# Kernel tuning notes

Hardware: AMD Instinct MI355X
Metric: run time of the kernel (lower is better)

Reference implementation:

```python
import jax, jax.numpy as jnp
import numpy as np

N_NODES = 150000
M_HYPEREDGES = 50000
N_TOTAL = N_NODES + M_HYPEREDGES
LATENT_DIM = 64
NUM_CLASS = 50
NNZ = 3_200_000
NUM_LAYERS = 3


def setup_inputs() -> dict:
    key = jax.random.key(0)
    k1, k2, k3, k4, k5, k6 = jax.random.split(key, 6)
    node_emb = 0.1 * jax.random.normal(k1, (N_NODES, LATENT_DIM), dtype=jnp.float32)
    hyper_emb = 0.1 * jax.random.normal(k2, (M_HYPEREDGES, LATENT_DIM), dtype=jnp.float32)
    W = jax.random.normal(k3, (LATENT_DIM, NUM_CLASS), dtype=jnp.float32) / np.sqrt(LATENT_DIM)
    b = jnp.zeros((NUM_CLASS,), dtype=jnp.float32)
    rows = jax.random.randint(k4, (NNZ,), 0, N_TOTAL, dtype=jnp.int32)
    cols = jax.random.randint(k5, (NNZ,), 0, N_TOTAL, dtype=jnp.int32)
    # normalized-adjacency-like small positive values
    vals = jax.random.uniform(k6, (NNZ,), dtype=jnp.float32) * 0.1
    return {"node_emb": node_emb, "hyper_emb": hyper_emb, "W": W, "b": b,
            "vals": vals, "rows": rows, "cols": cols}


def _spmm(vals, rows, cols, x):
    # y[r] = sum over edges (r, c): vals * x[c]   -- COO SpMM
    return jax.ops.segment_sum(vals[:, None] * x[cols], rows, num_segments=N_TOTAL)


def reference(node_emb, hyper_emb, W, b, vals, rows, cols):
    all_emb = jnp.concatenate([node_emb, hyper_emb], axis=0)  # [N, D]
    acc = all_emb  # running sum across layer embeddings (fused mean-pool)
    for _ in range(NUM_LAYERS):
        all_emb = _spmm(vals, rows, cols, all_emb)
        acc = acc + all_emb
    out = acc / (NUM_LAYERS + 1)          # mean over stacked layer embeddings
    nodes = out[:N_NODES]                 # split(out, [n_nodes, m_hyperedges])[0]
    Z = nodes @ W + b                     # linear head; dropout is identity in eval
    return jax.nn.log_softmax(Z, axis=1)
```

## Files before the change

kernel.cpp:

```cpp
#include <hip/hip_runtime.h>
#include <hip/hip_bf16.h>

#define N_NODES 150000
#define M_HYPER 50000
#define N_TOTAL 200000
#define DIM 64
#define NCLASS 50
#define NNZ 3200000

#define BSHIFT 9
#define BROWS 512
#define NBUK ((N_TOTAL + BROWS - 1) / BROWS)
#define EB 8192
#define CAP 9216

#define SCALE_UP 64.0f
#define SCALE_DN 0.015625f
#define VQ_ENC 163840.0f
#define VQ_DEC 6.103515625e-6f

#define SWZ(i) ((i) + ((i) >> 5))
#define SE_WORDS (CAP + CAP / 32)

typedef float v2f __attribute__((ext_vector_type(2)));

__global__ __launch_bounds__(1024) void bin_edges(
    const int* __restrict__ rows, const int* __restrict__ cols,
    const float* __restrict__ vals, int* __restrict__ bcur,
    int2* __restrict__ recs) {
    __shared__ int2 stage[EB];
    __shared__ int h[NBUK];
    __shared__ int lsb[NBUK];
    __shared__ int lb[NBUK];
    __shared__ int ps[512];
    int t = threadIdx.x;
    int base = blockIdx.x * EB;
    int cntE = NNZ - base; if (cntE > EB) cntE = EB;
    for (int i = t; i < NBUK; i += 1024) h[i] = 0;
    __syncthreads();
    for (int i = t; i < cntE; i += 1024)
        atomicAdd(&h[rows[base + i] >> BSHIFT], 1);
    __syncthreads();
    if (t < 512) ps[t] = (t < NBUK) ? h[t] : 0;
    __syncthreads();
    for (int off = 1; off < 512; off <<= 1) {
        int v = 0;
        if (t < 512 && t >= off) v = ps[t - off];
        __syncthreads();
        if (t < 512) ps[t] += v;
        __syncthreads();
    }
    if (t < NBUK) {
        int c = h[t];
        lsb[t] = ps[t] - c;
        lb[t] = t * CAP + (c ? atomicAdd(&bcur[t], c) : 0);
    }
    __syncthreads();
    for (int i = t; i < NBUK; i += 1024) h[i] = 0;
    __syncthreads();
    for (int i = t; i < cntE; i += 1024) {
        int e = base + i;
        int r = rows[e];
        int b = r >> BSHIFT;
        int q = __float2int_rn(vals[e] * VQ_ENC);
        if (q > 16383) q = 16383;
        int p = lsb[b] + atomicAdd(&h[b], 1);
        stage[p] = make_int2((int)(((unsigned)r << 14) | (unsigned)q), cols[e]);
    }
    __syncthreads();
    for (int i = t; i < cntE; i += 1024) {
        int2 rc = stage[i];
        int b = (int)((unsigned)rc.x >> 14) >> BSHIFT;
        int dst = lb[b] + (i - lsb[b]);
        if (dst < NBUK * CAP) recs[dst] = rc;
    }
}

__global__ __launch_bounds__(512) void cnt_scan(const int* __restrict__ bcur,
                                                int* __restrict__ boff) {
    __shared__ int sh[512];
    int t = threadIdx.x;
    int c = (t < NBUK) ? bcur[t] : 0;
    sh[t] = c;
    __syncthreads();
    for (int off = 1; off < 512; off <<= 1) {
        int v = (t >= off) ? sh[t - off] : 0;
        __syncthreads();
        sh[t] += v;
        __syncthreads();
    }
    if (t < NBUK) boff[t] = sh[t] - c;
    if (t == 0) boff[NBUK] = NNZ;
}

__global__ __launch_bounds__(512) void build_csr(const int* __restrict__ boff,
                                                 const int2* __restrict__ recs,
                                                 int* __restrict__ row_ptr,
                                                 unsigned* __restrict__ edges) {
    __shared__ int h[BROWS * 8];
    __shared__ int ps[512];
    __shared__ unsigned se[SE_WORDS];
    int b = blockIdx.x, t = threadIdx.x;
    int rbase = b * CAP;
    int obase = boff[b];
    int cnt = boff[b + 1] - obase;
    int row0 = b << BSHIFT;
    int nrows = N_TOTAL - row0;
    if (nrows > BROWS) nrows = BROWS;
    for (int i = t; i < BROWS * 8; i += 512) h[i] = 0;
    __syncthreads();
    for (int i = t; i < cnt; i += 512) {
        int2 rc = recs[rbase + i];
        int rrel = (int)(((unsigned)rc.x >> 14) & (BROWS - 1));
        int key = (rrel << 3) | (int)((unsigned)rc.y >> 15);
        atomicAdd(&h[key], 1);
    }
    __syncthreads();
    int loc[8];
    int s = 0;
#pragma unroll
    for (int j = 0; j < 8; ++j) { loc[j] = h[8 * t + j]; s += loc[j]; }
    ps[t] = s;
    __syncthreads();
    for (int off = 1; off < 512; off <<= 1) {
        int a = (t >= off) ? ps[t - off] : 0;
        __syncthreads();
        ps[t] += a;
        __syncthreads();
    }
    int run = (t == 0) ? 0 : ps[t - 1];
    if (t < nrows) row_ptr[row0 + t] = obase + run;
    if (b == NBUK - 1 && t == 0) row_ptr[N_TOTAL] = NNZ;
#pragma unroll
    for (int j = 0; j < 8; ++j) { h[8 * t + j] = run; run += loc[j]; }
    __syncthreads();
    for (int i = t; i < cnt; i += 512) {
        int2 rc = recs[rbase + i];
        unsigned rx = (unsigned)rc.x;
        int rrel = (int)((rx >> 14) & (BROWS - 1));
        int key = (rrel << 3) | (int)((unsigned)rc.y >> 15);
        int p = atomicAdd(&h[key], 1);
        se[SWZ(p)] = (unsigned)rc.y | ((rx & 0x3FFFu) << 18);
    }
    __syncthreads();
    for (int i = t; i < cnt; i += 512) edges[obase + i] = se[SWZ(i)];
}

__global__ __launch_bounds__(256) void sort_rows(const int* __restrict__ row_ptr,
                                                 unsigned* __restrict__ edges) {
    int row = blockIdx.x * 256 + threadIdx.x;
    if (row >= N_TOTAL) return;
    int beg = row_ptr[row], end = row_ptr[row + 1];
    int cnt = end - beg;
    if (cnt <= 1) return;
    if (cnt <= 32) {
        unsigned v[32];
#pragma unroll
        for (int i = 0; i < 32; ++i)
            v[i] = (i < cnt) ? edges[beg + i] : 0xFFFFFFFFu;
#pragma unroll
        for (int k = 2; k <= 32; k <<= 1) {
#pragma unroll
            for (int j = k >> 1; j > 0; j >>= 1) {
#pragma unroll
                for (int i = 0; i < 32; ++i) {
                    int l = i ^ j;
                    if (l > i) {
                        bool up = ((i & k) == 0);
                        unsigned a = v[i], c = v[l];
                        bool sw = up ? (a > c) : (a < c);
                        v[i] = sw ? c : a;
                        v[l] = sw ? a : c;
                    }
                }
            }
        }
#pragma unroll
        for (int i = 0; i < 32; ++i)
            if (i < cnt) edges[beg + i] = v[i];
    } else {
        for (int i = 1; i < cnt; ++i) {
            unsigned key = edges[beg + i];
            int j = i - 1;
            while (j >= 0 && edges[beg + j] > key) {
                edges[beg + j + 1] = edges[beg + j];
                --j;
            }
            edges[beg + j + 1] = key;
        }
    }
}

__global__ __launch_bounds__(256) void build_x_fp8(
    const float* __restrict__ node_emb, const float* __restrict__ hyper_emb,
    unsigned* __restrict__ xb) {
    int i = blockIdx.x * 256 + threadIdx.x;
    size_t base = (size_t)i * 4;
    const size_t NN = (size_t)N_NODES * DIM;
    if (base >= (size_t)N_TOTAL * DIM) return;
    float4 f;
    if (base < NN)
        f = *reinterpret_cast<const float4*>(node_emb + base);
    else
        f = *reinterpret_cast<const float4*>(hyper_emb + (base - NN));
    int lo = __builtin_amdgcn_cvt_pk_fp8_f32(f.x * SCALE_UP, f.y * SCALE_UP,
                                             0, false);
    int w = __builtin_amdgcn_cvt_pk_fp8_f32(f.z * SCALE_UP, f.w * SCALE_UP,
                                            lo, true);
    xb[i] = (unsigned)w;
}

__global__ __launch_bounds__(256) void spmm_gather(
    const int* __restrict__ row_ptr, const unsigned* __restrict__ edges,
    const unsigned char* __restrict__ x, unsigned char* __restrict__ y,
    int nrows) {
    int gid = blockIdx.x * 256 + threadIdx.x;
    int row = gid >> 4;
    int lane = threadIdx.x & 15;
    if (row >= nrows) return;
    int beg = row_ptr[row], end = row_ptr[row + 1];
    float a0 = 0.f, a1 = 0.f, a2 = 0.f, a3 = 0.f;
    int k = beg;
    for (; k + 7 < end; k += 8) {
        unsigned e[8];
        unsigned g[8];
#pragma unroll
        for (int j = 0; j < 8; ++j) e[j] = edges[k + j];
#pragma unroll
        for (int j = 0; j < 8; ++j)
            g[j] = *(const unsigned*)(x + ((size_t)(e[j] & 0x3FFFFu) << 6) + lane * 4);
#pragma unroll
        for (int j = 0; j < 8; ++j) {
            float v = (float)(e[j] >> 18) * VQ_DEC;
            v2f lo = __builtin_amdgcn_cvt_pk_f32_fp8((int)g[j], false);
            v2f hi = __builtin_amdgcn_cvt_pk_f32_fp8((int)g[j], true);
            a0 = fmaf(v, lo[0], a0);
            a1 = fmaf(v, lo[1], a1);
            a2 = fmaf(v, hi[0], a2);
            a3 = fmaf(v, hi[1], a3);
        }
    }
    for (; k + 3 < end; k += 4) {
        unsigned e[4];
        unsigned g[4];
#pragma unroll
        for (int j = 0; j < 4; ++j) e[j] = edges[k + j];
#pragma unroll
        for (int j = 0; j < 4; ++j)
            g[j] = *(const unsigned*)(x + ((size_t)(e[j] & 0x3FFFFu) << 6) + lane * 4);
#pragma unroll
        for (int j = 0; j < 4; ++j) {
            float v = (float)(e[j] >> 18) * VQ_DEC;
            v2f lo = __builtin_amdgcn_cvt_pk_f32_fp8((int)g[j], false);
            v2f hi = __builtin_amdgcn_cvt_pk_f32_fp8((int)g[j], true);
            a0 = fmaf(v, lo[0], a0);
            a1 = fmaf(v, lo[1], a1);
            a2 = fmaf(v, hi[0], a2);
            a3 = fmaf(v, hi[1], a3);
        }
    }
    for (; k < end; ++k) {
        unsigned e = edges[k];
        unsigned g = *(const unsigned*)(x + ((size_t)(e & 0x3FFFFu) << 6) + lane * 4);
        float v = (float)(e >> 18) * VQ_DEC;
        v2f lo = __builtin_amdgcn_cvt_pk_f32_fp8((int)g, false);
        v2f hi = __builtin_amdgcn_cvt_pk_f32_fp8((int)g, true);
        a0 = fmaf(v, lo[0], a0);
        a1 = fmaf(v, lo[1], a1);
        a2 = fmaf(v, hi[0], a2);
        a3 = fmaf(v, hi[1], a3);
    }
    int plo = __builtin_amdgcn_cvt_pk_fp8_f32(a0, a1, 0, false);
    int pk = __builtin_amdgcn_cvt_pk_fp8_f32(a2, a3, plo, true);
    *(unsigned*)(y + ((size_t)row << 6) + lane * 4) = (unsigned)pk;
}

__global__ __launch_bounds__(256) void classify(
    const float* __restrict__ node_emb, const unsigned char* __restrict__ y1,
    const unsigned char* __restrict__ y2,
    const unsigned char* __restrict__ y3, const float* __restrict__ W,
    const float* __restrict__ bias, float* __restrict__ Z) {
    __shared__ float zl[256 * 51];
    int t = threadIdx.x;
    int block_base = blockIdx.x * 256;
    int row = block_base + t;
    if (row < N_NODES) {
        const float4* np =
            reinterpret_cast<const float4*>(node_emb + (size_t)row * DIM);
        const unsigned* p1 = (const unsigned*)(y1 + ((size_t)row << 6));
        const unsigned* p2 = (const unsigned*)(y2 + ((size_t)row << 6));
        const unsigned* p3 = (const unsigned*)(y3 + ((size_t)row << 6));
        float xr[DIM];
#pragma unroll
        for (int i = 0; i < DIM / 4; ++i) {
            float4 f = np[i];
            unsigned w1 = p1[i], w2 = p2[i], w3 = p3[i];
            v2f a0 = __builtin_amdgcn_cvt_pk_f32_fp8((int)w1, false);
            v2f a1 = __builtin_amdgcn_cvt_pk_f32_fp8((int)w1, true);
            v2f b0 = __builtin_amdgcn_cvt_pk_f32_fp8((int)w2, false);
            v2f b1 = __builtin_amdgcn_cvt_pk_f32_fp8((int)w2, true);
            v2f c0 = __builtin_amdgcn_cvt_pk_f32_fp8((int)w3, false);
            v2f c1 = __builtin_amdgcn_cvt_pk_f32_fp8((int)w3, true);
            xr[4 * i + 0] = (f.x + (a0[0] + b0[0] + c0[0]) * SCALE_DN) * 0.25f;
            xr[4 * i + 1] = (f.y + (a0[1] + b0[1] + c0[1]) * SCALE_DN) * 0.25f;
            xr[4 * i + 2] = (f.z + (a1[0] + b1[0] + c1[0]) * SCALE_DN) * 0.25f;
            xr[4 * i + 3] = (f.w + (a1[1] + b1[1] + c1[1]) * SCALE_DN) * 0.25f;
        }
        float m = -1e30f;
#pragma unroll 1
        for (int c = 0; c < NCLASS; ++c) {
            float d0 = bias[c], d1 = 0.f;
#pragma unroll
            for (int k = 0; k < DIM; k += 2) {
                d0 = fmaf(xr[k + 0], W[(k + 0) * NCLASS + c], d0);
                d1 = fmaf(xr[k + 1], W[(k + 1) * NCLASS + c], d1);
            }
            float d = d0 + d1;
            zl[t * 51 + c] = d;
            m = fmaxf(m, d);
        }
        float s = 0.f;
#pragma unroll 1
        for (int c = 0; c < NCLASS; ++c) s += __expf(zl[t * 51 + c] - m);
        float ls = m + __logf(s);
#pragma unroll 1
        for (int c = 0; c < NCLASS; ++c) zl[t * 51 + c] -= ls;
    }
    __syncthreads();
    int n_valid = N_NODES - block_base;
    if (n_valid > 256) n_valid = 256;
    if (n_valid < 0) n_valid = 0;
    int total = n_valid * NCLASS;
    float* zbase = Z + (size_t)block_base * NCLASS;
    for (int i = t; i < total; i += 256) {
        int r = i / NCLASS;
        int c = i - r * NCLASS;
        zbase[i] = zl[r * 51 + c];
    }
}

extern "C" void kernel_launch(void* const* d_in, const int* in_sizes, int n_in,
                              void* d_out, int out_size, void* d_ws, size_t ws_size,
                              hipStream_t stream) {
    const float* node_emb = (const float*)d_in[0];
    const float* hyper_emb = (const float*)d_in[1];
    const float* W = (const float*)d_in[2];
    const float* b = (const float*)d_in[3];
    const float* vals = (const float*)d_in[4];
    const int* rows = (const int*)d_in[5];
    const int* cols = (const int*)d_in[6];
    float* Z = (float*)d_out;

    const size_t BUF8 = (size_t)N_TOTAL * DIM;
    const size_t EDG = (size_t)NNZ * 4;

    char* w = (char*)d_ws;
    unsigned char* xb = (unsigned char*)w;  w += BUF8;
    unsigned char* y1 = (unsigned char*)w;  w += BUF8;
    unsigned char* y2 = (unsigned char*)w;  w += BUF8;
    unsigned char* y3 = (unsigned char*)w;  w += BUF8;
    unsigned* edges = (unsigned*)w;         w += EDG;
    int* row_ptr = (int*)w;                 w += (size_t)(N_TOTAL + 1) * 4;
    int* boff = (int*)w;                    w += 2048;
    int* bcur = (int*)w;                    w += 2048;
    int2* recs = (int2*)w;

    hipMemsetAsync(bcur, 0, NBUK * 4, stream);
    const int bin_blocks = (NNZ + EB - 1) / EB;
    bin_edges<<<bin_blocks, 1024, 0, stream>>>(rows, cols, vals, bcur, recs);
    cnt_scan<<<1, 512, 0, stream>>>(bcur, boff);
    build_csr<<<NBUK, 512, 0, stream>>>(boff, recs, row_ptr, edges);
    sort_rows<<<(N_TOTAL + 255) / 256, 256, 0, stream>>>(row_ptr, edges);

    const int cvt_blocks = (int)(((size_t)N_TOTAL * DIM / 4 + 255) / 256);
    build_x_fp8<<<cvt_blocks, 256, 0, stream>>>(node_emb, hyper_emb,
                                                (unsigned*)xb);

    const int out_blocks = (N_NODES + 255) / 256;
    const int full_blocks = (N_TOTAL * 16 + 255) / 256;
    const int node_blocks = (N_NODES * 16 + 255) / 256;

    spmm_gather<<<full_blocks, 256, 0, stream>>>(row_ptr, edges, xb, y1,
                                                 N_TOTAL);
    spmm_gather<<<full_blocks, 256, 0, stream>>>(row_ptr, edges, y1, y2,
                                                 N_TOTAL);
    spmm_gather<<<node_blocks, 256, 0, stream>>>(row_ptr, edges, y2, y3,
                                                 N_NODES);
    classify<<<out_blocks, 256, 0, stream>>>(node_emb, y1, y2, y3, W, b, Z);
}
```

Before: 325.5 us.

## Sort CSR rows with 32-lane warp-shuffle bitonic network instead of per-thread

Replaces the one-thread-per-row register bitonic sort with 32 lanes per row that sort via cross-lane shuffle exchanges. This removes the large per-thread register array and long serial compare chain, and gives coalesced loads and stores of each row's edges. The cost is 32x more threads launched, and the rare rows longer than 32 still fall back to a single-lane insertion sort. Shuffles use width 64, so each 64-wide wavefront holds two row groups.

```diff
diff --git a/kernel.cpp b/kernel.cpp
--- a/kernel.cpp
+++ b/kernel.cpp
@@ -148,37 +148,28 @@
 
 __global__ __launch_bounds__(256) void sort_rows(const int* __restrict__ row_ptr,
                                                  unsigned* __restrict__ edges) {
-    int row = blockIdx.x * 256 + threadIdx.x;
+    int gid = blockIdx.x * 256 + threadIdx.x;
+    int row = gid >> 5;
+    int lane = threadIdx.x & 31;
     if (row >= N_TOTAL) return;
     int beg = row_ptr[row], end = row_ptr[row + 1];
     int cnt = end - beg;
-    if (cnt <= 1) return;
+    unsigned v = (lane < cnt) ? edges[beg + lane] : 0xFFFFFFFFu;
+#pragma unroll
+    for (int k = 2; k <= 32; k <<= 1) {
+#pragma unroll
+        for (int j = k >> 1; j > 0; j >>= 1) {
+            unsigned o = __shfl_xor(v, j, 64);
+            bool up = ((lane & k) == 0);
+            bool lower = ((lane & j) == 0);
+            unsigned mn = v < o ? v : o;
+            unsigned mx = v < o ? o : v;
+            v = (up == lower) ? mn : mx;
+        }
+    }
     if (cnt <= 32) {
-        unsigned v[32];
-#pragma unroll
-        for (int i = 0; i < 32; ++i)
-            v[i] = (i < cnt) ? edges[beg + i] : 0xFFFFFFFFu;
-#pragma unroll
-        for (int k = 2; k <= 32; k <<= 1) {
-#pragma unroll
-            for (int j = k >> 1; j > 0; j >>= 1) {
-#pragma unroll
-                for (int i = 0; i < 32; ++i) {
-                    int l = i ^ j;
-                    if (l > i) {
-                        bool up = ((i & k) == 0);
-                        unsigned a = v[i], c = v[l];
-                        bool sw = up ? (a > c) : (a < c);
-                        v[i] = sw ? c : a;
-                        v[l] = sw ? a : c;
-                    }
-                }
-            }
-        }
-#pragma unroll
-        for (int i = 0; i < 32; ++i)
-            if (i < cnt) edges[beg + i] = v[i];
-    } else {
+        if (lane < cnt && cnt > 1) edges[beg + lane] = v;
+    } else if (lane == 0) {
         for (int i = 1; i < cnt; ++i) {
             unsigned key = edges[beg + i];
             int j = i - 1;
@@ -370,7 +361,7 @@
     bin_edges<<<bin_blocks, 1024, 0, stream>>>(rows, cols, vals, bcur, recs);
     cnt_scan<<<1, 512, 0, stream>>>(bcur, boff);
     build_csr<<<NBUK, 512, 0, stream>>>(boff, recs, row_ptr, edges);
-    sort_rows<<<(N_TOTAL + 255) / 256, 256, 0, stream>>>(row_ptr, edges);
+    sort_rows<<<(N_TOTAL * 32 + 255) / 256, 256, 0, stream>>>(row_ptr, edges);
 
     const int cvt_blocks = (int)(((size_t)N_TOTAL * DIM / 4 + 255) / 256);
     build_x_fp8<<<cvt_blocks, 256, 0, stream>>>(node_emb, hyper_emb,
```

New measurement: 329.7 us. No clear change (+1.3%).
